# Kernel optimization log

Hardware: AMD Instinct MI355X
Metric: run time of the kernel (lower is better)

The kernel has to match this reference:

```python
import jax, jax.numpy as jnp
import numpy as np

N_NODES = 50000


def setup_inputs() -> dict:
    key = jax.random.key(0)
    k1, k2, k3, k4, k5 = jax.random.split(key, 5)
    in_feats, out_feats = 64, 64
    n_edges = 800000
    feature = jax.random.normal(k1, (N_NODES, in_feats), dtype=jnp.float32)
    edge_src = jax.random.randint(k2, (n_edges,), 0, N_NODES, dtype=jnp.int64)
    edge_dst = jax.random.randint(k3, (n_edges,), 0, N_NODES, dtype=jnp.int64)
    # nn.Linear init scale ~ 1/sqrt(in_feats); plain normal is fine for a numeric reference
    W = jax.random.normal(k4, (out_feats, in_feats), dtype=jnp.float32) / jnp.sqrt(jnp.float32(in_feats))
    b = jax.random.normal(k5, (out_feats,), dtype=jnp.float32) * 0.01
    return {"feature": feature, "edge_src": edge_src, "edge_dst": edge_dst, "W": W, "b": b}


def reference(feature, edge_src, edge_dst, W, b):
    # msg = copy_src('h'): gather src features along edges -> [E, F]
    msgs = feature[edge_src]
    # reduce = mean over mailbox: segment-mean by destination node
    agg = jax.ops.segment_sum(msgs, edge_dst, num_segments=N_NODES)  # [N, F]
    cnt = jax.ops.segment_sum(jnp.ones((edge_src.shape[0],), dtype=feature.dtype),
                              edge_dst, num_segments=N_NODES)  # [N]
    mean = agg / jnp.maximum(cnt, 1.0)[:, None]
    # DGL: nodes with no incoming messages keep their original feature 'h'
    h = jnp.where(cnt[:, None] > 0, mean, feature)
    # apply_nodes: ReLU(W h + b) on all nodes
    return jax.nn.relu(h @ W.T + b)
```

## Files before the change

kernel.cpp:

```cpp
#include <hip/hip_runtime.h>


#define F 64
#define CAP 48
#define SHW 256
#define EB 2048
#define OVF_MAX 32768

typedef unsigned int uint;
typedef unsigned short ushort;

__device__ __forceinline__ ushort f2bf(float x) {
    uint u = __float_as_uint(x);
    u += 0x7FFFu + ((u >> 16) & 1u);
    return (ushort)(u >> 16);
}

__global__ __launch_bounds__(256) void k_work(const float* __restrict__ feature,
                                              const float* __restrict__ W,
                                              ushort* __restrict__ Ybf,
                                              const int* __restrict__ esrc,
                                              const int* __restrict__ edst,
                                              int* __restrict__ blkBuf,
                                              int* __restrict__ pfxTab,
                                              int* __restrict__ ovfB,
                                              int N, int E, int G) {
    __shared__ alignas(16) char smem[28672];
    int tid = threadIdx.x, bid = blockIdx.x;
    if (bid == 0 && tid == 0) ovfB[0] = 0;

    if (bid < G) {
        float* sWt = (float*)smem;
        float* shh = (float*)(smem + 19456);
        for (int i = tid; i < 4096; i += 256) {
            int fo = i >> 6, k = i & 63;
            sWt[k * 76 + fo] = W[i];
        }
        int n0blk = bid * 32;
        for (int i = tid; i < 512; i += 256) {
            int r = i >> 4, c4 = i & 15;
            int n = n0blk + r;
            float4 v = make_float4(0.f, 0.f, 0.f, 0.f);
            if (n < N) v = ((const float4*)feature)[(long)n * 16 + c4];
            *(float4*)&shh[r * 72 + c4 * 4] = v;
        }
        __syncthreads();
        int npair = tid >> 4, foq = tid & 15;
        int r0 = npair * 2, r1 = r0 + 1;
        float a0=0,a1=0,a2=0,a3=0,b0=0,b1=0,b2=0,b3=0;
#pragma unroll 8
        for (int k = 0; k < 64; ++k) {
            float hA = shh[r0 * 72 + k];
            float hB = shh[r1 * 72 + k];
            float4 wv = *(const float4*)&sWt[k * 76 + foq * 4];
            a0 = fmaf(hA, wv.x, a0); a1 = fmaf(hA, wv.y, a1);
            a2 = fmaf(hA, wv.z, a2); a3 = fmaf(hA, wv.w, a3);
            b0 = fmaf(hB, wv.x, b0); b1 = fmaf(hB, wv.y, b1);
            b2 = fmaf(hB, wv.z, b2); b3 = fmaf(hB, wv.w, b3);
        }
        int nA = n0blk + r0, nB = n0blk + r1;
        if (nA < N) ((ushort4*)Ybf)[(long)nA * 16 + foq] =
            make_ushort4(f2bf(a0), f2bf(a1), f2bf(a2), f2bf(a3));
        if (nB < N) ((ushort4*)Ybf)[(long)nB * 16 + foq] =
            make_ushort4(f2bf(b0), f2bf(b1), f2bf(b2), f2bf(b3));
    } else {
        int* cnt   = (int*)smem;
        int* sc    = (int*)(smem + 1024);
        int* pfx   = (int*)(smem + 2048);
        int* off   = (int*)(smem + 3072);
        int* stage = (int*)(smem + 4096);

        int b = bid - G;
        int ebase = b * EB;
        int d[8], s[8];
        int i0 = ebase + tid * 8;
        if (i0 + 7 < E) {
            int4 a  = *(const int4*)(edst + i0);
            int4 b4 = *(const int4*)(edst + i0 + 4);
            d[0]=a.x; d[1]=a.y; d[2]=a.z; d[3]=a.w;
            d[4]=b4.x; d[5]=b4.y; d[6]=b4.z; d[7]=b4.w;
            int4 c4 = *(const int4*)(esrc + i0);
            int4 e4 = *(const int4*)(esrc + i0 + 4);
            s[0]=c4.x; s[1]=c4.y; s[2]=c4.z; s[3]=c4.w;
            s[4]=e4.x; s[5]=e4.y; s[6]=e4.z; s[7]=e4.w;
        } else {
#pragma unroll
            for (int k = 0; k < 8; ++k) {
                int e = i0 + k;
                d[k] = (e < E) ? edst[e] : -1;
                s[k] = (e < E) ? esrc[e] : 0;
            }
        }
        cnt[tid] = 0;
        __syncthreads();
#pragma unroll
        for (int k = 0; k < 8; ++k)
            if (d[k] >= 0) atomicAdd(&cnt[d[k] >> 8], 1);
        __syncthreads();
        int own = cnt[tid];
        sc[tid] = own;
        __syncthreads();
        for (int dd = 1; dd < 256; dd <<= 1) {
            int t = (tid >= dd) ? sc[tid - dd] : 0;
            __syncthreads();
            sc[tid] += t;
            __syncthreads();
        }
        pfx[tid] = sc[tid] - own;
        off[tid] = sc[tid] - own;
        __syncthreads();
#pragma unroll
        for (int k = 0; k < 8; ++k) {
            if (d[k] >= 0) {
                int sh = d[k] >> 8;
                int sl = atomicAdd(&off[sh], 1);
                stage[sl] = ((d[k] & 255) << 24) | s[k];
            }
        }
        __syncthreads();
        int total = pfx[255] + cnt[255];
        for (int i = tid; i < total; i += 256)
            blkBuf[ebase + i] = stage[i];
        pfxTab[b * 257 + tid] = pfx[tid];
        if (tid == 0) pfxTab[b * 257 + 256] = total;
    }
}

__global__ __launch_bounds__(1024) void k_bingather(const ushort* __restrict__ Ybf,
                                                    const int* __restrict__ blkBuf,
                                                    const int* __restrict__ pfxTab,
                                                    int* __restrict__ ovfB,
                                                    const float* __restrict__ bias,
                                                    float* __restrict__ out,
                                                    int N, int S) {
    __shared__ int dl[SHW];
    __shared__ int bl[SHW * CAP];
    int tid = threadIdx.x;
    int sh  = blockIdx.x;
    for (int i = tid; i < SHW; i += 1024) dl[i] = 0;
    __syncthreads();
    for (int b = tid; b < S; b += 1024) {
        int lo = pfxTab[b * 257 + sh];
        int hi = pfxTab[b * 257 + sh + 1];
        for (int i = lo; i < hi; ++i) {
            int v = blkBuf[b * EB + i];
            int lid = ((uint)v) >> 24;
            int s = v & 0xFFFFFF;
            int r = atomicAdd(&dl[lid], 1);
            if (r < CAP) bl[lid * CAP + r] = s;
            else { int o = atomicAdd(&ovfB[0], 1);
                   if (o < OVF_MAX) { ovfB[2 + 2*o] = sh * SHW + lid; ovfB[3 + 2*o] = s; } }
        }
    }
    __syncthreads();
    int wv = tid >> 6, lane = tid & 63;
    int g = lane >> 3, c = lane & 7;
    const uint4* Y16 = (const uint4*)Ybf;
    for (int pass = 0; pass < SHW / 16; ++pass) {
        int lid = pass * 16 + wv;
        int n = sh * SHW + lid;
        if (n < N) {
            int d = dl[lid];
            int m = min(d, CAP);
            float acc[4][8];
#pragma unroll
            for (int ch = 0; ch < 4; ++ch)
#pragma unroll
                for (int j = 0; j < 8; ++j) acc[ch][j] = 0.f;
            int last = m - 1;
            for (int base = 0; base < m; base += 32) {
#pragma unroll
                for (int ch = 0; ch < 4; ++ch) {
                    int jdx = base + ch * 8 + g;
                    int s = bl[lid * CAP + min(jdx, last)];
                    uint4 q = Y16[(long)s * 8 + c];
                    if (jdx < m) {
                        acc[ch][0] += __uint_as_float(q.x << 16);
                        acc[ch][1] += __uint_as_float(q.x & 0xFFFF0000u);
                        acc[ch][2] += __uint_as_float(q.y << 16);
                        acc[ch][3] += __uint_as_float(q.y & 0xFFFF0000u);
                        acc[ch][4] += __uint_as_float(q.z << 16);
                        acc[ch][5] += __uint_as_float(q.z & 0xFFFF0000u);
                        acc[ch][6] += __uint_as_float(q.w << 16);
                        acc[ch][7] += __uint_as_float(q.w & 0xFFFF0000u);
                    }
                }
            }
            if (d > CAP) {
                int no = ovfB[0]; if (no > OVF_MAX) no = OVF_MAX;
                if (g == 0) {
                    for (int i = 0; i < no; ++i) {
                        if (ovfB[2 + 2*i] == n) {
                            int s = ovfB[3 + 2*i];
                            uint4 q = Y16[(long)s * 8 + c];
                            acc[0][0] += __uint_as_float(q.x << 16);
                            acc[0][1] += __uint_as_float(q.x & 0xFFFF0000u);
                            acc[0][2] += __uint_as_float(q.y << 16);
                            acc[0][3] += __uint_as_float(q.y & 0xFFFF0000u);
                            acc[0][4] += __uint_as_float(q.z << 16);
                            acc[0][5] += __uint_as_float(q.z & 0xFFFF0000u);
                            acc[0][6] += __uint_as_float(q.w << 16);
                            acc[0][7] += __uint_as_float(q.w & 0xFFFF0000u);
                        }
                    }
                }
            }
#pragma unroll
            for (int j = 0; j < 8; ++j)
                acc[0][j] += (acc[1][j] + acc[2][j]) + acc[3][j];
#pragma unroll
            for (int j = 0; j < 8; ++j) {
                float v = acc[0][j];
                v += __shfl_xor(v, 8);
                v += __shfl_xor(v, 16);
                v += __shfl_xor(v, 32);
                acc[0][j] = v;
            }
            float sel = acc[0][0];
#pragma unroll
            for (int j = 1; j < 8; ++j) sel = (g == j) ? acc[0][j] : sel;
            int fw = c * 8 + g;
            float hv;
            if (d > 0) hv = sel / (float)d;
            else       hv = __uint_as_float(((uint)Ybf[(long)n * F + fw]) << 16);
            out[(long)n * F + fw] = fmaxf(hv + bias[fw], 0.0f);
        }
    }
}

__global__ __launch_bounds__(256) void k_gemm13(const float* __restrict__ feature,
                                                const float* __restrict__ W,
                                                ushort* __restrict__ Ybf, int N,
                                                int* __restrict__ deg, int n4,
                                                int* __restrict__ ovfB) {
    {
        int gt = blockIdx.x * 256 + threadIdx.x;
        if (gt == 0) ovfB[0] = 0;
        for (int i = gt; i < n4; i += gridDim.x * 256)
            ((int4*)deg)[i] = make_int4(0, 0, 0, 0);
    }
    __shared__ float sWt[64 * 76];
    __shared__ float shh[32 * 72];
    int tid = threadIdx.x;
    for (int i = tid; i < 4096; i += 256) {
        int fo = i >> 6, k = i & 63;
        sWt[k * 76 + fo] = W[i];
    }
    int n0blk = blockIdx.x * 32;
    for (int i = tid; i < 512; i += 256) {
        int r = i >> 4, c4 = i & 15;
        int n = n0blk + r;
        float4 v = make_float4(0.f, 0.f, 0.f, 0.f);
        if (n < N) v = ((const float4*)feature)[(long)n * 16 + c4];
        *(float4*)&shh[r * 72 + c4 * 4] = v;
    }
    __syncthreads();
    int npair = tid >> 4, foq = tid & 15;
    int r0 = npair * 2, r1 = r0 + 1;
    float a0=0,a1=0,a2=0,a3=0,b0=0,b1=0,b2=0,b3=0;
#pragma unroll 8
    for (int k = 0; k < 64; ++k) {
        float hA = shh[r0 * 72 + k];
        float hB = shh[r1 * 72 + k];
        float4 wv = *(const float4*)&sWt[k * 76 + foq * 4];
        a0 = fmaf(hA, wv.x, a0); a1 = fmaf(hA, wv.y, a1);
        a2 = fmaf(hA, wv.z, a2); a3 = fmaf(hA, wv.w, a3);
        b0 = fmaf(hB, wv.x, b0); b1 = fmaf(hB, wv.y, b1);
        b2 = fmaf(hB, wv.z, b2); b3 = fmaf(hB, wv.w, b3);
    }
    int nA = n0blk + r0, nB = n0blk + r1;
    if (nA < N) ((ushort4*)Ybf)[(long)nA * 16 + foq] =
        make_ushort4(f2bf(a0), f2bf(a1), f2bf(a2), f2bf(a3));
    if (nB < N) ((ushort4*)Ybf)[(long)nB * 16 + foq] =
        make_ushort4(f2bf(b0), f2bf(b1), f2bf(b2), f2bf(b3));
}

__global__ __launch_bounds__(256) void k_scatter13(const int* __restrict__ esrc,
                                                   const int* __restrict__ edst,
                                                   int* __restrict__ deg,
                                                   int* __restrict__ bucket,
                                                   int* __restrict__ ovfB, int E) {
    int base = (blockIdx.x * 256 + threadIdx.x) * 4;
    if (base + 3 < E) {
        int4 d4 = *(const int4*)(edst + base);
        int4 s4 = *(const int4*)(esrc + base);
        int r0 = atomicAdd(&deg[d4.x], 1);
        int r1 = atomicAdd(&deg[d4.y], 1);
        int r2 = atomicAdd(&deg[d4.z], 1);
        int r3 = atomicAdd(&deg[d4.w], 1);
        if (r0 < CAP) bucket[d4.x * CAP + r0] = s4.x;
        else { int o = atomicAdd(&ovfB[0], 1); if (o < OVF_MAX) { ovfB[2 + 2*o] = d4.x; ovfB[3 + 2*o] = s4.x; } }
        if (r1 < CAP) bucket[d4.y * CAP + r1] = s4.y;
        else { int o = atomicAdd(&ovfB[0], 1); if (o < OVF_MAX) { ovfB[2 + 2*o] = d4.y; ovfB[3 + 2*o] = s4.y; } }
        if (r2 < CAP) bucket[d4.z * CAP + r2] = s4.z;
        else { int o = atomicAdd(&ovfB[0], 1); if (o < OVF_MAX) { ovfB[2 + 2*o] = d4.z; ovfB[3 + 2*o] = s4.z; } }
        if (r3 < CAP) bucket[d4.w * CAP + r3] = s4.w;
        else { int o = atomicAdd(&ovfB[0], 1); if (o < OVF_MAX) { ovfB[2 + 2*o] = d4.w; ovfB[3 + 2*o] = s4.w; } }
    } else {
        for (int e = base; e < E; ++e) {
            int d = edst[e], s = esrc[e];
            int r = atomicAdd(&deg[d], 1);
            if (r < CAP) bucket[d * CAP + r] = s;
            else { int o = atomicAdd(&ovfB[0], 1); if (o < OVF_MAX) { ovfB[2 + 2*o] = d; ovfB[3 + 2*o] = s; } }
        }
    }
}

__global__ __launch_bounds__(256) void k_gatherG(const ushort* __restrict__ Ybf,
                                                 const int* __restrict__ deg,
                                                 const int* __restrict__ bucket,
                                                 const int* __restrict__ ovf,
                                                 const float* __restrict__ bias,
                                                 float* __restrict__ out, int N) {
    int tid = threadIdx.x;
    int w = tid >> 6, lane = tid & 63;
    int g = lane >> 3, c = lane & 7;
    int n = blockIdx.x * 4 + w;
    if (n >= N) return;
    int d = deg[n];
    int m = min(d, CAP);
    int boff = n * CAP;
    const uint4* Y16 = (const uint4*)Ybf;
    float acc[4][8];
#pragma unroll
    for (int ch = 0; ch < 4; ++ch)
#pragma unroll
        for (int j = 0; j < 8; ++j) acc[ch][j] = 0.f;
    int last = m - 1;
    for (int base = 0; base < m; base += 32) {
#pragma unroll
        for (int ch = 0; ch < 4; ++ch) {
            int jdx = base + ch * 8 + g;
            int s = bucket[boff + min(jdx, last)];
            uint4 q = Y16[(long)s * 8 + c];
            if (jdx < m) {
                acc[ch][0] += __uint_as_float(q.x << 16);
                acc[ch][1] += __uint_as_float(q.x & 0xFFFF0000u);
                acc[ch][2] += __uint_as_float(q.y << 16);
                acc[ch][3] += __uint_as_float(q.y & 0xFFFF0000u);
                acc[ch][4] += __uint_as_float(q.z << 16);
                acc[ch][5] += __uint_as_float(q.z & 0xFFFF0000u);
                acc[ch][6] += __uint_as_float(q.w << 16);
                acc[ch][7] += __uint_as_float(q.w & 0xFFFF0000u);
            }
        }
    }
    if (d > CAP) {
        int no = ovf[0]; if (no > OVF_MAX) no = OVF_MAX;
        if (g == 0) {
            for (int i = 0; i < no; ++i) {
                if (ovf[2 + 2*i] == n) {
                    int s = ovf[3 + 2*i];
                    uint4 q = Y16[(long)s * 8 + c];
                    acc[0][0] += __uint_as_float(q.x << 16);
                    acc[0][1] += __uint_as_float(q.x & 0xFFFF0000u);
                    acc[0][2] += __uint_as_float(q.y << 16);
                    acc[0][3] += __uint_as_float(q.y & 0xFFFF0000u);
                    acc[0][4] += __uint_as_float(q.z << 16);
                    acc[0][5] += __uint_as_float(q.z & 0xFFFF0000u);
                    acc[0][6] += __uint_as_float(q.w << 16);
                    acc[0][7] += __uint_as_float(q.w & 0xFFFF0000u);
                }
            }
        }
    }
#pragma unroll
    for (int j = 0; j < 8; ++j)
        acc[0][j] += (acc[1][j] + acc[2][j]) + acc[3][j];
#pragma unroll
    for (int j = 0; j < 8; ++j) {
        float v = acc[0][j];
        v += __shfl_xor(v, 8);
        v += __shfl_xor(v, 16);
        v += __shfl_xor(v, 32);
        acc[0][j] = v;
    }
    float sel = acc[0][0];
#pragma unroll
    for (int j = 1; j < 8; ++j) sel = (g == j) ? acc[0][j] : sel;
    int fw = c * 8 + g;
    float hv;
    if (d > 0) hv = sel / (float)d;
    else       hv = __uint_as_float(((uint)Ybf[(long)n * F + fw]) << 16);
    out[(long)n * F + fw] = fmaxf(hv + bias[fw], 0.0f);
}

__global__ __launch_bounds__(256) void gcn_edge_scatter(const float* __restrict__ feature,
                                                        const int* __restrict__ esrc,
                                                        const int* __restrict__ edst,
                                                        float* __restrict__ agg,
                                                        float* __restrict__ cnt, int E) {
    int t = blockIdx.x * blockDim.x + threadIdx.x;
    int e = t >> 6, f = t & 63;
    if (e >= E) return;
    atomicAdd(&agg[(long)edst[e] * F + f], feature[(long)esrc[e] * F + f]);
    if (f == 0) atomicAdd(&cnt[edst[e]], 1.0f);
}
__global__ __launch_bounds__(256) void gcn_node_apply(const float* __restrict__ feature,
                                                      const float* __restrict__ W,
                                                      const float* __restrict__ bias,
                                                      const float* __restrict__ cnt,
                                                      float* __restrict__ inout, int N) {
    __shared__ float sWt[64 * 65];
    __shared__ float sh[4][64];
    int tid = threadIdx.x;
    for (int i = tid; i < 64 * 64; i += 256) {
        int fo = i >> 6, k = i & 63;
        sWt[k * 65 + fo] = W[i];
    }
    int w = tid >> 6, f = tid & 63;
    int n = blockIdx.x * 4 + w;
    float h = 0.0f;
    if (n < N) {
        float c = cnt[n];
        h = (c > 0.0f) ? inout[(long)n * F + f] / c : feature[(long)n * F + f];
    }
    sh[w][f] = h;
    __syncthreads();
    float acc = bias[f];
#pragma unroll
    for (int k = 0; k < 64; ++k) acc = fmaf(sh[w][k], sWt[k * 65 + f], acc);
    if (n < N) inout[(long)n * F + f] = fmaxf(acc, 0.0f);
}

extern "C" void kernel_launch(void* const* d_in, const int* in_sizes, int n_in,
                              void* d_out, int out_size, void* d_ws, size_t ws_size,
                              hipStream_t stream) {
    const float* feature = (const float*)d_in[0];
    const int*   esrc    = (const int*)d_in[1];
    const int*   edst    = (const int*)d_in[2];
    const float* W       = (const float*)d_in[3];
    const float* bias    = (const float*)d_in[4];

    int N = in_sizes[0] / F;
    int E = in_sizes[1];

    int G   = (N + 31) / 32;
    int S   = (E + EB - 1) / EB;
    int NSH = (N + SHW - 1) / SHW;

    auto align256 = [](size_t x) { return (x + 255) & ~(size_t)255; };
    size_t sz_ovf = align256((2 + 2 * (size_t)OVF_MAX) * sizeof(int));
    size_t sz_Y   = align256((size_t)N * F * sizeof(ushort));
    size_t sz_blk = align256((size_t)S * EB * sizeof(int));
    size_t sz_pfx = align256((size_t)S * 257 * sizeof(int));
    size_t need_new = sz_ovf + sz_Y + sz_blk + sz_pfx;

    size_t sz_deg    = align256((size_t)N * sizeof(int));
    size_t sz_bucket = align256((size_t)N * CAP * sizeof(int));
    size_t need_mid  = sz_ovf + sz_Y + sz_deg + sz_bucket;

    if (ws_size >= need_new && N <= 65536) {
        char* ws = (char*)d_ws;
        int*    ovfB   = (int*)ws;    ws += sz_ovf;
        ushort* Ybf    = (ushort*)ws; ws += sz_Y;
        int*    blkBuf = (int*)ws;    ws += sz_blk;
        int*    pfxTab = (int*)ws;
        float*  out    = (float*)d_out;

        k_work<<<G + S, 256, 0, stream>>>(feature, W, Ybf, esrc, edst,
                                          blkBuf, pfxTab, ovfB, N, E, G);
        k_bingather<<<NSH, 1024, 0, stream>>>(Ybf, blkBuf, pfxTab, ovfB,
                                              bias, out, N, S);
    } else if (ws_size >= need_mid) {
        char* ws = (char*)d_ws;
        int*    ovfB   = (int*)ws;    ws += sz_ovf;
        ushort* Ybf    = (ushort*)ws; ws += sz_Y;
        int*    deg    = (int*)ws;    ws += sz_deg;
        int*    bucket = (int*)ws;
        float*  out    = (float*)d_out;
        int n4 = (N + 3) / 4;
        int gE4 = (E + 1023) / 1024;

        k_gemm13<<<G, 256, 0, stream>>>(feature, W, Ybf, N, deg, n4, ovfB);
        k_scatter13<<<gE4, 256, 0, stream>>>(esrc, edst, deg, bucket, ovfB, E);
        k_gatherG<<<(N + 3) / 4, 256, 0, stream>>>(Ybf, deg, bucket, ovfB, bias, out, N);
    } else {
        float* agg = (float*)d_out;
        float* cnt = (float*)d_ws;
        hipMemsetAsync(agg, 0, (size_t)N * F * sizeof(float), stream);
        hipMemsetAsync(cnt, 0, (size_t)N * sizeof(float), stream);
        long total = (long)E * F;
        gcn_edge_scatter<<<(int)((total + 255) / 256), 256, 0, stream>>>(
            feature, esrc, edst, agg, cnt, E);
        gcn_node_apply<<<(N + 3) / 4, 256, 0, stream>>>(feature, W, bias, cnt, agg, N);
    }
}
```

Baseline: 63.53 us.

## Split each bin-gather shard across four 256-thread blocks by quarter

The bin-gather kernel previously ran one 1024-thread block per 256-node shard with a 48KB shared bucket. Each shard is now handled by four 256-thread blocks, each owning a 64-node quarter and filtering bin entries by quarter. This cuts shared memory per block and raises block count, which should improve occupancy and load balance across CUs. In exchange every block rescans the shard's whole bin list, so bin reads from global memory increase fourfold.

```diff
diff --git a/kernel.cpp b/kernel.cpp
--- a/kernel.cpp
+++ b/kernel.cpp
@@ -4,6 +4,7 @@
 #define F 64
 #define CAP 48
 #define SHW 256
+#define QW 64
 #define EB 2048
 #define OVF_MAX 32768
 
@@ -126,41 +127,45 @@
     }
 }
 
-__global__ __launch_bounds__(1024) void k_bingather(const ushort* __restrict__ Ybf,
-                                                    const int* __restrict__ blkBuf,
-                                                    const int* __restrict__ pfxTab,
-                                                    int* __restrict__ ovfB,
-                                                    const float* __restrict__ bias,
-                                                    float* __restrict__ out,
-                                                    int N, int S) {
-    __shared__ int dl[SHW];
-    __shared__ int bl[SHW * CAP];
+__global__ __launch_bounds__(256) void k_bingather(const ushort* __restrict__ Ybf,
+                                                   const int* __restrict__ blkBuf,
+                                                   const int* __restrict__ pfxTab,
+                                                   int* __restrict__ ovfB,
+                                                   const float* __restrict__ bias,
+                                                   float* __restrict__ out,
+                                                   int N, int S) {
+    __shared__ int dl[QW];
+    __shared__ int bl[QW * CAP];
     int tid = threadIdx.x;
-    int sh  = blockIdx.x;
-    for (int i = tid; i < SHW; i += 1024) dl[i] = 0;
+    int sh  = blockIdx.x >> 2;
+    int q   = blockIdx.x & 3;
+    for (int i = tid; i < QW; i += 256) dl[i] = 0;
     __syncthreads();
-    for (int b = tid; b < S; b += 1024) {
+    for (int b = tid; b < S; b += 256) {
         int lo = pfxTab[b * 257 + sh];
         int hi = pfxTab[b * 257 + sh + 1];
         for (int i = lo; i < hi; ++i) {
             int v = blkBuf[b * EB + i];
             int lid = ((uint)v) >> 24;
-            int s = v & 0xFFFFFF;
-            int r = atomicAdd(&dl[lid], 1);
-            if (r < CAP) bl[lid * CAP + r] = s;
-            else { int o = atomicAdd(&ovfB[0], 1);
-                   if (o < OVF_MAX) { ovfB[2 + 2*o] = sh * SHW + lid; ovfB[3 + 2*o] = s; } }
+            if ((lid >> 6) == q) {
+                int ll = lid & 63;
+                int s = v & 0xFFFFFF;
+                int r = atomicAdd(&dl[ll], 1);
+                if (r < CAP) bl[ll * CAP + r] = s;
+                else { int o = atomicAdd(&ovfB[0], 1);
+                       if (o < OVF_MAX) { ovfB[2 + 2*o] = sh * SHW + lid; ovfB[3 + 2*o] = s; } }
+            }
         }
     }
     __syncthreads();
     int wv = tid >> 6, lane = tid & 63;
     int g = lane >> 3, c = lane & 7;
     const uint4* Y16 = (const uint4*)Ybf;
-    for (int pass = 0; pass < SHW / 16; ++pass) {
-        int lid = pass * 16 + wv;
-        int n = sh * SHW + lid;
+    for (int pass = 0; pass < QW / 4; ++pass) {
+        int ll = pass * 4 + wv;
+        int n = sh * SHW + q * QW + ll;
         if (n < N) {
-            int d = dl[lid];
+            int d = dl[ll];
             int m = min(d, CAP);
             float acc[4][8];
 #pragma unroll
@@ -172,17 +177,17 @@
 #pragma unroll
                 for (int ch = 0; ch < 4; ++ch) {
                     int jdx = base + ch * 8 + g;
-                    int s = bl[lid * CAP + min(jdx, last)];
-                    uint4 q = Y16[(long)s * 8 + c];
+                    int s = bl[ll * CAP + min(jdx, last)];
+                    uint4 qv = Y16[(long)s * 8 + c];
                     if (jdx < m) {
-                        acc[ch][0] += __uint_as_float(q.x << 16);
-                        acc[ch][1] += __uint_as_float(q.x & 0xFFFF0000u);
-                        acc[ch][2] += __uint_as_float(q.y << 16);
-                        acc[ch][3] += __uint_as_float(q.y & 0xFFFF0000u);
-                        acc[ch][4] += __uint_as_float(q.z << 16);
-                        acc[ch][5] += __uint_as_float(q.z & 0xFFFF0000u);
-                        acc[ch][6] += __uint_as_float(q.w << 16);
-                        acc[ch][7] += __uint_as_float(q.w & 0xFFFF0000u);
+                        acc[ch][0] += __uint_as_float(qv.x << 16);
+                        acc[ch][1] += __uint_as_float(qv.x & 0xFFFF0000u);
+                        acc[ch][2] += __uint_as_float(qv.y << 16);
+                        acc[ch][3] += __uint_as_float(qv.y & 0xFFFF0000u);
+                        acc[ch][4] += __uint_as_float(qv.z << 16);
+                        acc[ch][5] += __uint_as_float(qv.z & 0xFFFF0000u);
+                        acc[ch][6] += __uint_as_float(qv.w << 16);
+                        acc[ch][7] += __uint_as_float(qv.w & 0xFFFF0000u);
                     }
                 }
             }
@@ -192,15 +197,15 @@
                     for (int i = 0; i < no; ++i) {
                         if (ovfB[2 + 2*i] == n) {
                             int s = ovfB[3 + 2*i];
-                            uint4 q = Y16[(long)s * 8 + c];
-                            acc[0][0] += __uint_as_float(q.x << 16);
-                            acc[0][1] += __uint_as_float(q.x & 0xFFFF0000u);
-                            acc[0][2] += __uint_as_float(q.y << 16);
-                            acc[0][3] += __uint_as_float(q.y & 0xFFFF0000u);
-                            acc[0][4] += __uint_as_float(q.z << 16);
-                            acc[0][5] += __uint_as_float(q.z & 0xFFFF0000u);
-                            acc[0][6] += __uint_as_float(q.w << 16);
-                            acc[0][7] += __uint_as_float(q.w & 0xFFFF0000u);
+                            uint4 qv = Y16[(long)s * 8 + c];
+                            acc[0][0] += __uint_as_float(qv.x << 16);
+                            acc[0][1] += __uint_as_float(qv.x & 0xFFFF0000u);
+                            acc[0][2] += __uint_as_float(qv.y << 16);
+                            acc[0][3] += __uint_as_float(qv.y & 0xFFFF0000u);
+                            acc[0][4] += __uint_as_float(qv.z << 16);
+                            acc[0][5] += __uint_as_float(qv.z & 0xFFFF0000u);
+                            acc[0][6] += __uint_as_float(qv.w << 16);
+                            acc[0][7] += __uint_as_float(qv.w & 0xFFFF0000u);
                         }
                     }
                 }
@@ -332,16 +337,16 @@
         for (int ch = 0; ch < 4; ++ch) {
             int jdx = base + ch * 8 + g;
             int s = bucket[boff + min(jdx, last)];
-            uint4 q = Y16[(long)s * 8 + c];
+            uint4 qv = Y16[(long)s * 8 + c];
             if (jdx < m) {
-                acc[ch][0] += __uint_as_float(q.x << 16);
-                acc[ch][1] += __uint_as_float(q.x & 0xFFFF0000u);
-                acc[ch][2] += __uint_as_float(q.y << 16);
-                acc[ch][3] += __uint_as_float(q.y & 0xFFFF0000u);
-                acc[ch][4] += __uint_as_float(q.z << 16);
-                acc[ch][5] += __uint_as_float(q.z & 0xFFFF0000u);
-                acc[ch][6] += __uint_as_float(q.w << 16);
-                acc[ch][7] += __uint_as_float(q.w & 0xFFFF0000u);
+                acc[ch][0] += __uint_as_float(qv.x << 16);
+                acc[ch][1] += __uint_as_float(qv.x & 0xFFFF0000u);
+                acc[ch][2] += __uint_as_float(qv.y << 16);
+                acc[ch][3] += __uint_as_float(qv.y & 0xFFFF0000u);
+                acc[ch][4] += __uint_as_float(qv.z << 16);
+                acc[ch][5] += __uint_as_float(qv.z & 0xFFFF0000u);
+                acc[ch][6] += __uint_as_float(qv.w << 16);
+                acc[ch][7] += __uint_as_float(qv.w & 0xFFFF0000u);
             }
         }
     }
@@ -351,15 +356,15 @@
             for (int i = 0; i < no; ++i) {
                 if (ovf[2 + 2*i] == n) {
                     int s = ovf[3 + 2*i];
-                    uint4 q = Y16[(long)s * 8 + c];
-                    acc[0][0] += __uint_as_float(q.x << 16);
-                    acc[0][1] += __uint_as_float(q.x & 0xFFFF0000u);
-                    acc[0][2] += __uint_as_float(q.y << 16);
-                    acc[0][3] += __uint_as_float(q.y & 0xFFFF0000u);
-                    acc[0][4] += __uint_as_float(q.z << 16);
-                    acc[0][5] += __uint_as_float(q.z & 0xFFFF0000u);
-                    acc[0][6] += __uint_as_float(q.w << 16);
-                    acc[0][7] += __uint_as_float(q.w & 0xFFFF0000u);
+                    uint4 qv = Y16[(long)s * 8 + c];
+                    acc[0][0] += __uint_as_float(qv.x << 16);
+                    acc[0][1] += __uint_as_float(qv.x & 0xFFFF0000u);
+                    acc[0][2] += __uint_as_float(qv.y << 16);
+                    acc[0][3] += __uint_as_float(qv.y & 0xFFFF0000u);
+                    acc[0][4] += __uint_as_float(qv.z << 16);
+                    acc[0][5] += __uint_as_float(qv.z & 0xFFFF0000u);
+                    acc[0][6] += __uint_as_float(qv.w << 16);
+                    acc[0][7] += __uint_as_float(qv.w & 0xFFFF0000u);
                 }
             }
         }
@@ -460,8 +465,8 @@
 
         k_work<<<G + S, 256, 0, stream>>>(feature, W, Ybf, esrc, edst,
                                           blkBuf, pfxTab, ovfB, N, E, G);
-        k_bingather<<<NSH, 1024, 0, stream>>>(Ybf, blkBuf, pfxTab, ovfB,
-                                              bias, out, N, S);
+        k_bingather<<<NSH * 4, 256, 0, stream>>>(Ybf, blkBuf, pfxTab, ovfB,
+                                                 bias, out, N, S);
     } else if (ws_size >= need_mid) {
         char* ws = (char*)d_ws;
         int*    ovfB   = (int*)ws;    ws += sz_ovf;
```

After: 72.96 us. 1.15x slower.
